# Optimization experiments

Measured on AMD Instinct MI355X. Metric: run time of the kernel, lower is better.

## Reference

```python
import jax, jax.numpy as jnp
import numpy as np

E_IN = 1 << 20   # input events
E_OUT = 1 << 17  # output events (= len(times_out))
K = 9            # kernel_size (temporal taps)
C_IN = 64        # filters_in
C_OUT = 64       # filters


def setup_inputs() -> dict:
    key = jax.random.key(0)
    ks = jax.random.split(key, 6)
    features = jax.random.normal(ks[0], (E_IN, C_IN), jnp.float32)
    dt = jax.random.uniform(ks[1], (E_IN,), jnp.float32)          # time since event, >= 0
    times_out = jax.random.uniform(ks[2], (E_OUT,), jnp.float32)  # only its length is used
    successor_kernel_ids = jax.random.randint(ks[3], (E_IN,), 0, K, jnp.int32)
    segment_ids_out = jax.random.randint(ks[4], (E_IN,), 0, E_OUT, jnp.int32)
    # parameters per build(): decay_rate (C_in,) zeros-init, kernel glorot, bias zeros
    decay_rate = jnp.zeros((C_IN,), jnp.float32)
    glorot = float(np.sqrt(2.0 / (C_IN + C_OUT)))
    kernel = jax.random.normal(ks[5], (K, C_IN, C_OUT), jnp.float32) * glorot
    bias = jnp.zeros((C_OUT,), jnp.float32)
    return dict(features=features, dt=dt, times_out=times_out,
                decay_rate=decay_rate, kernel=kernel, bias=bias,
                successor_kernel_ids=successor_kernel_ids,
                segment_ids_out=segment_ids_out)


def reference(features, dt, times_out, decay_rate, kernel, bias,
              successor_kernel_ids, segment_ids_out):
    """ExclusiveConv forward: exp-decay weighting, per-kernel-tap segment sum,
    normalization by summed decay weights, small kernel matmul, bias.
    normalize=True, activation=None, decay_rate_activation=softplus."""
    k, c_in, c_out = kernel.shape
    e_out = times_out.shape[0]
    rate = jax.nn.softplus(decay_rate)                       # [C_in]
    w = jnp.exp(-dt[:, None] * rate[None, :])                # [E_in, C_in] decay weights
    vals = w * features                                      # [E_in, C_in]
    # each input event goes exclusively to (output event, kernel tap)
    seg = segment_ids_out.astype(jnp.int32) * k + successor_kernel_ids  # [E_in]
    num = jax.ops.segment_sum(vals, seg, num_segments=e_out * k)        # [E_out*K, C_in]
    den = jax.ops.segment_sum(w, seg, num_segments=e_out * k)           # [E_out*K, C_in]
    agg = jnp.where(den > 0, num / jnp.where(den > 0, den, 1.0), 0.0)   # normalized
    agg = agg.reshape(e_out, k, c_in)
    out = jnp.einsum('ekc,kcf->ef', agg, kernel) + bias      # [E_out, C_out]
    return out
```

## Files before the change

kernel.cpp:

```cpp
#include <hip/hip_runtime.h>
#include <hip/hip_bf16.h>
#include <stdint.h>

#define E_IN_N   1048576
#define E_OUT_N  131072
#define KTAPS    9
#define CIN      64
#define COUT     64
#define NCELL    (E_OUT_N*KTAPS)
#define NB_SCAN  1152
#define TILE_E   32
#define NKSTEP   18

typedef __attribute__((ext_vector_type(8))) short bf16x8;
typedef __attribute__((ext_vector_type(4))) float f32x4;

__device__ __forceinline__ ushort f32_bf16(float x){
  union{float f; uint32_t u;} v; v.f=x;
  uint32_t r = v.u + 0x7FFFu + ((v.u>>16)&1u);
  return (ushort)(r>>16);
}

__global__ void zero_k(int* __restrict__ p){
  int i = blockIdx.x*256 + threadIdx.x;
  ((int4*)p)[i] = int4{0,0,0,0};
}

__global__ void hist_k(const int* __restrict__ seg, const int* __restrict__ succ,
                       int* __restrict__ counts, uint32_t* __restrict__ cellrank){
  int i = blockIdx.x*256 + threadIdx.x;
  uint32_t cell = (uint32_t)(seg[i]*KTAPS + succ[i]);
  uint32_t rank = (uint32_t)atomicAdd(&counts[cell],1);
  cellrank[i] = (cell<<11) | rank;
}

__global__ void blocksum_k(const int* __restrict__ counts, int* __restrict__ bsum){
  __shared__ int sm[256];
  int b=blockIdx.x, t=threadIdx.x;
  const int4 c4 = *(const int4*)(counts + b*1024 + t*4);
  int s=c4.x+c4.y+c4.z+c4.w;
  sm[t]=s; __syncthreads();
  for(int d=128; d>0; d>>=1){ if(t<d) sm[t]+=sm[t+d]; __syncthreads(); }
  if(t==0) bsum[b]=sm[0];
}

__global__ void offsets_k(const int* __restrict__ counts, const int* __restrict__ bsum,
                          int* __restrict__ offsets){
  __shared__ int sm[256];
  int b=blockIdx.x, t=threadIdx.x;
  int s=0;
  for(int j=t; j<NB_SCAN; j+=256) if(j<b) s+=bsum[j];
  sm[t]=s; __syncthreads();
  for(int d=128; d>0; d>>=1){ if(t<d) sm[t]+=sm[t+d]; __syncthreads(); }
  int base0=sm[0]; __syncthreads();
  int base=b*1024+t*4;
  const int4 c4=*(const int4*)(counts+base);
  int s2=c4.x+c4.y+c4.z+c4.w;
  sm[t]=s2; __syncthreads();
  for(int d=1; d<256; d<<=1){ int x=(t>=d)?sm[t-d]:0; __syncthreads(); sm[t]+=x; __syncthreads(); }
  int e0v=base0 + ((t==0)?0:sm[t-1]);
  int4 o; o.x=e0v; o.y=e0v+c4.x; o.z=o.y+c4.y; o.w=o.z+c4.z;
  *(int4*)(offsets+base)=o;
  if(b==NB_SCAN-1 && t==255) offsets[NCELL]=o.w+c4.w;
}

__global__ void scatter_k(const uint32_t* __restrict__ cellrank, const float* __restrict__ dtv,
                          const int* __restrict__ offsets, int2* __restrict__ sorted2){
  int i=blockIdx.x*256+threadIdx.x;
  uint32_t cr=cellrank[i];
  uint32_t cell=cr>>11, rank=cr&2047u;
  int base=offsets[cell];
  float d=dtv[i];
  uint32_t x=cell>>5;
  uint32_t q=__umulhi(x,477218592u);
  uint32_t rel=cell - q*288u;
  sorted2[base+(int)rank]=int2{(int)((uint32_t)i | (rel<<20)), __float_as_int(d)};
}

__global__ void wprep_k(const float* __restrict__ wk, ushort* __restrict__ wb){
  int slot=blockIdx.x*256+threadIdx.x;
  int j=slot&7; int t2=slot>>3; int lane=t2&63; int t3=t2>>6;
  int ks=t3%NKSTEP; int nt=t3/NKSTEP;
  int r=ks*32+((lane>>4)*8)+j; int col=nt*16+(lane&15);
  wb[slot]=f32_bf16(wk[r*COUT+col]);
}

#define ISSUE(Fb,bb) { \
  _Pragma("unroll") \
  for(int u=0;u<8;u++){ \
    int e=(bb)*8+u; int ec=(e<cn)?e:(cn-1); \
    int iu=__shfl(pw,ec)&0xFFFFF; \
    (Fb)[u]=features[((size_t)iu<<6)+lane]; } }

#define FLUSH { int le=(curRel*7282)>>16; int kk=curRel-le*9; \
  float rr=__builtin_amdgcn_rcpf(den); \
  agg[le*584+kk*64+lane]=f32_bf16(num*rr); }

#define CONSUME(Fb,bb) { \
  _Pragma("unroll") \
  for(int u=0;u<8;u++){ \
    int e=(bb)*8+u; \
    if(e<cn){ \
      int r_=__shfl(pw,e)>>20; float d_=__shfl(pd,e); \
      if(r_!=curRel){ \
        if(curRel>=0){ FLUSH } \
        curRel=r_; num=0.f; den=0.f; } \
      float w=__expf(-d_*rate); \
      num=fmaf(w,(Fb)[u],num); den+=w; } } }

__global__ __launch_bounds__(512,4) void compute_k(
    const float* __restrict__ features, const float* __restrict__ decay,
    const float* __restrict__ bias, const int* __restrict__ offsets,
    const int2* __restrict__ sorted2, const ushort* __restrict__ wb,
    float* __restrict__ out)
{
  __shared__ ushort agg[TILE_E*584];
  const int tid=threadIdx.x, wv=tid>>6, lane=tid&63;
  const int e0=blockIdx.x*TILE_E;
  const int cb0=e0*KTAPS;

  for(int i=tid;i<TILE_E*584/2;i+=512) ((uint32_t*)agg)[i]=0u;
  float x=decay[lane];
  float rate=fmaxf(x,0.f)+log1pf(__expf(-fabsf(x)));
  __syncthreads();

  {
    const int c0=cb0+wv*36;
    int jv=0; if(lane<2) jv=offsets[c0+lane*36];
    const int j0=__shfl(jv,0), jEnd=__shfl(jv,1);
    int curRel=-1; float num=0.f, den=0.f;

    if(j0<jEnd){
      int2 P=sorted2[min(j0+lane,jEnd-1)];
      for(int cb=j0; cb<jEnd; cb+=64){
        const int cn=min(64,jEnd-cb);
        int nx=cb+64+lane;
        int2 Pn=sorted2[(nx<jEnd)?nx:(jEnd-1)];
        const int pw=P.x; const float pd=__int_as_float(P.y);
        const int nb=(cn+7)>>3;
        float Af[8],Bf[8];
        ISSUE(Af,0)
        if(nb>1) ISSUE(Bf,1)
        CONSUME(Af,0)
        if(nb>2) ISSUE(Af,2)
        if(nb>1) CONSUME(Bf,1)
        if(nb>3) ISSUE(Bf,3)
        if(nb>2) CONSUME(Af,2)
        if(nb>4) ISSUE(Af,4)
        if(nb>3) CONSUME(Bf,3)
        if(nb>5) ISSUE(Bf,5)
        if(nb>4) CONSUME(Af,4)
        if(nb>6) ISSUE(Af,6)
        if(nb>5) CONSUME(Bf,5)
        if(nb>7) ISSUE(Bf,7)
        if(nb>6) CONSUME(Af,6)
        if(nb>7) CONSUME(Bf,7)
        P=Pn;
      }
      if(curRel>=0){ FLUSH }
    }
  }
  __syncthreads();

  const int mt=wv>>2, nt=wv&3;
  const int arow=mt*16+(lane&15);
  const int koff=(lane>>4)*8;
  const ushort* wbp = wb + ((size_t)(nt*NKSTEP)*64 + (size_t)lane)*8;
  f32x4 acc={0.f,0.f,0.f,0.f};
  #pragma unroll
  for(int ks=0;ks<NKSTEP;ks++){
    bf16x8 a=*(const bf16x8*)&agg[arow*584+ks*32+koff];
    bf16x8 bfr=*(const bf16x8*)(wbp + (size_t)ks*512);
    acc=__builtin_amdgcn_mfma_f32_16x16x32_bf16(a,bfr,acc,0,0,0);
  }
  const int orow=e0+mt*16+((lane>>4)*4);
  const int ocol=nt*16+(lane&15);
  const float bv=bias[ocol];
  #pragma unroll
  for(int r=0;r<4;r++) out[(size_t)(orow+r)*COUT+ocol]=acc[r]+bv;
}

extern "C" void kernel_launch(void* const* d_in, const int* in_sizes, int n_in,
                              void* d_out, int out_size, void* d_ws, size_t ws_size,
                              hipStream_t stream){
  const float* features=(const float*)d_in[0];
  const float* dtv=(const float*)d_in[1];
  const float* decay=(const float*)d_in[3];
  const float* wk=(const float*)d_in[4];
  const float* bias=(const float*)d_in[5];
  const int* succ=(const int*)d_in[6];
  const int* seg=(const int*)d_in[7];

  char* ws=(char*)d_ws;
  size_t o=0;
  int* counts=(int*)(ws+o);      o+=(size_t)NCELL*4;
  int* offsets=(int*)(ws+o);     o+=(size_t)(NCELL+4)*4;
  int* bsum=(int*)(ws+o);        o+=(size_t)NB_SCAN*4;
  uint32_t* cellrank=(uint32_t*)(ws+o); o+=(size_t)E_IN_N*4;
  int2* sorted2=(int2*)(ws+o);   o+=(size_t)E_IN_N*8;
  ushort* wb=(ushort*)(ws+o);    o+=(size_t)36864*2;
  float* out=(float*)d_out;

  hipLaunchKernelGGL(zero_k, dim3(NCELL/1024),dim3(256),0,stream, counts);
  hipLaunchKernelGGL(hist_k, dim3(E_IN_N/256),dim3(256),0,stream, seg,succ,counts,cellrank);
  hipLaunchKernelGGL(blocksum_k, dim3(NB_SCAN),dim3(256),0,stream, counts,bsum);
  hipLaunchKernelGGL(offsets_k, dim3(NB_SCAN),dim3(256),0,stream, counts,bsum,offsets);
  hipLaunchKernelGGL(scatter_k, dim3(E_IN_N/256),dim3(256),0,stream, cellrank,dtv,offsets,sorted2);
  hipLaunchKernelGGL(wprep_k, dim3(144),dim3(256),0,stream, wk,wb);
  hipLaunchKernelGGL(compute_k, dim3(E_OUT_N/TILE_E),dim3(512),0,stream,
                     features,decay,bias,offsets,sorted2,wb,out);
}
```

Before: 210.2 us.

## Replace shuffle-based gather loop with branchless uniform 16-event batches

The per-wave aggregation loop no longer loads 64 sorted entries per lane and broadcasts them with shuffles. Each lane now reads the same 16 sorted entries through wave-uniform loads, gathers 16 feature rows, and accumulates them without branches. Segment changes reset the running sums by multiplying with a select, and the normalized value is written to shared memory after every event, so the explicit flush path goes away. This trims shuffle and divergence overhead and raises the number of loads in flight, at the cost of redundant shared-memory stores and reads up to 15 entries past the range, which needs the padded workspace.

```diff
diff --git a/kernel.cpp b/kernel.cpp
--- a/kernel.cpp
+++ b/kernel.cpp
@@ -85,29 +85,6 @@
   wb[slot]=f32_bf16(wk[r*COUT+col]);
 }
 
-#define ISSUE(Fb,bb) { \
-  _Pragma("unroll") \
-  for(int u=0;u<8;u++){ \
-    int e=(bb)*8+u; int ec=(e<cn)?e:(cn-1); \
-    int iu=__shfl(pw,ec)&0xFFFFF; \
-    (Fb)[u]=features[((size_t)iu<<6)+lane]; } }
-
-#define FLUSH { int le=(curRel*7282)>>16; int kk=curRel-le*9; \
-  float rr=__builtin_amdgcn_rcpf(den); \
-  agg[le*584+kk*64+lane]=f32_bf16(num*rr); }
-
-#define CONSUME(Fb,bb) { \
-  _Pragma("unroll") \
-  for(int u=0;u<8;u++){ \
-    int e=(bb)*8+u; \
-    if(e<cn){ \
-      int r_=__shfl(pw,e)>>20; float d_=__shfl(pd,e); \
-      if(r_!=curRel){ \
-        if(curRel>=0){ FLUSH } \
-        curRel=r_; num=0.f; den=0.f; } \
-      float w=__expf(-d_*rate); \
-      num=fmaf(w,(Fb)[u],num); den+=w; } } }
-
 __global__ __launch_bounds__(512,4) void compute_k(
     const float* __restrict__ features, const float* __restrict__ decay,
     const float* __restrict__ bias, const int* __restrict__ offsets,
@@ -127,37 +104,40 @@
   {
     const int c0=cb0+wv*36;
     int jv=0; if(lane<2) jv=offsets[c0+lane*36];
-    const int j0=__shfl(jv,0), jEnd=__shfl(jv,1);
-    int curRel=-1; float num=0.f, den=0.f;
+    int cb = __builtin_amdgcn_readfirstlane(__shfl(jv,0));
+    const int jE = __builtin_amdgcn_readfirstlane(__shfl(jv,1));
 
-    if(j0<jEnd){
-      int2 P=sorted2[min(j0+lane,jEnd-1)];
-      for(int cb=j0; cb<jEnd; cb+=64){
-        const int cn=min(64,jEnd-cb);
-        int nx=cb+64+lane;
-        int2 Pn=sorted2[(nx<jEnd)?nx:(jEnd-1)];
-        const int pw=P.x; const float pd=__int_as_float(P.y);
-        const int nb=(cn+7)>>3;
-        float Af[8],Bf[8];
-        ISSUE(Af,0)
-        if(nb>1) ISSUE(Bf,1)
-        CONSUME(Af,0)
-        if(nb>2) ISSUE(Af,2)
-        if(nb>1) CONSUME(Bf,1)
-        if(nb>3) ISSUE(Bf,3)
-        if(nb>2) CONSUME(Af,2)
-        if(nb>4) ISSUE(Af,4)
-        if(nb>3) CONSUME(Bf,3)
-        if(nb>5) ISSUE(Bf,5)
-        if(nb>4) CONSUME(Af,4)
-        if(nb>6) ISSUE(Af,6)
-        if(nb>5) CONSUME(Bf,5)
-        if(nb>7) ISSUE(Bf,7)
-        if(nb>6) CONSUME(Af,6)
-        if(nb>7) CONSUME(Bf,7)
-        P=Pn;
+    int prevRel=-1;
+    float num=0.f, den=1.f;
+
+    while(cb<jE){
+      int qx[16]; float qd[16];
+      #pragma unroll
+      for(int e=0;e<16;e++){
+        int2 t=sorted2[cb+e];
+        qx[e]=t.x; qd[e]=__int_as_float(t.y);
       }
-      if(curRel>=0){ FLUSH }
+      float fl[16];
+      #pragma unroll
+      for(int e=0;e<16;e++){
+        int iu = qx[e] & 0xFFFFF;
+        fl[e] = features[((size_t)iu<<6) + lane];
+      }
+      #pragma unroll
+      for(int e=0;e<16;e++){
+        const int ok = (cb+e) < jE;
+        int rel = (int)(((uint32_t)qx[e])>>20);
+        rel = ok ? rel : prevRel;
+        float w = __expf(-qd[e]*rate);
+        w = ok ? w : 0.f;
+        const float same = (rel==prevRel) ? 1.f : 0.f;
+        num = num*same + w*fl[e];
+        den = den*same + w;
+        const int le=(rel*7282)>>16, kk=rel-le*9;
+        agg[le*584 + kk*64 + lane] = f32_bf16(num*__builtin_amdgcn_rcpf(den));
+        prevRel = rel;
+      }
+      cb += 16;
     }
   }
   __syncthreads();
@@ -197,7 +177,7 @@
   int* offsets=(int*)(ws+o);     o+=(size_t)(NCELL+4)*4;
   int* bsum=(int*)(ws+o);        o+=(size_t)NB_SCAN*4;
   uint32_t* cellrank=(uint32_t*)(ws+o); o+=(size_t)E_IN_N*4;
-  int2* sorted2=(int2*)(ws+o);   o+=(size_t)E_IN_N*8;
+  int2* sorted2=(int2*)(ws+o);   o+=(size_t)(E_IN_N+16)*8;
   ushort* wb=(ushort*)(ws+o);    o+=(size_t)36864*2;
   float* out=(float*)d_out;
 
```

New measurement: 175.2 us. -16.6%, faster.
